# Optimization experiments

Measured on AMD Instinct MI355X. Metric: run time of the kernel, lower is better.

Reference implementation:

```python
import jax, jax.numpy as jnp
import numpy as np

ALPHA = 0.1          # loss decay rate along the hierarchy
H = 8                # hierarchy depth
NUM_CLASSES = 10000
NUM_NODES = 15000
BATCH = 1024


def setup_inputs() -> dict:
    key = jax.random.key(0)
    k1, k2, k3, k4 = jax.random.split(key, 4)
    logits = jax.random.normal(k1, (BATCH, NUM_CLASSES), dtype=jnp.float32)
    target_classes = jax.random.randint(k2, (BATCH,), 0, NUM_CLASSES)
    # L is an integer node/leaf matrix; values drawn in {1, 2} to avoid
    # division-by-zero in the module's num/den ratio (torch casts L to int).
    L = jax.random.randint(k3, (NUM_NODES, NUM_CLASSES), 1, 3)
    path_to_root = jax.random.randint(k4, (NUM_CLASSES, H), 0, NUM_NODES)
    return {"logits": logits, "target_classes": target_classes,
            "L": L, "path_to_root": path_to_root}


def reference(logits, target_classes, L, path_to_root):
    # Faithful to the torch forward, including the inner-loop index i
    # shadowing the batch index (logits rows 0..H-3 are used for every
    # sample). The unused log_softmax dead code is omitted.
    B = logits.shape[0]
    steps = H - 2
    paths = path_to_root[target_classes]                     # (B, H)
    lam = jnp.exp(-ALPHA * (H - jnp.arange(steps, dtype=logits.dtype) - 1.0))  # (steps,)
    Lf = L.astype(logits.dtype)
    # gather hierarchy rows for each sample/step: (B, steps, C)
    num = Lf[paths[:, :steps]] * logits[None, :steps, :]
    den = Lf[paths[:, 1:steps + 1]] * logits[None, :steps, :]
    terms = lam[None, :, None] * (num / den)                 # (B, steps, C)
    return -terms.sum(axis=(0, 1)) / B                       # (C,)
```

## Files before the change

kernel.cpp:

```cpp
#include <hip/hip_runtime.h>

#define ALPHA 0.1f
#define HDEPTH 8
#define STEPS 6
#define NCLASS 10000
#define NNODES 15000
#define BATCH 1024
#define NPAIRS (BATCH * STEPS)

#define PACK_STRIDE 320
#define NCOLS 313
#define NGROUPS 157
#define CHUNK 64
#define NCHUNKS (NPAIRS / CHUNK)

__global__ void build_pairs_kernel(const int* __restrict__ target,
                                   const int* __restrict__ path,
                                   int2* __restrict__ pairs,
                                   unsigned char* __restrict__ flags) {
    int p = blockIdx.x * blockDim.x + threadIdx.x;
    if (p >= NPAIRS) return;
    int s = p >> 10;
    int b = p & (BATCH - 1);
    int t = target[b];
    int n1 = path[t * HDEPTH + s];
    int n2 = path[t * HDEPTH + s + 1];
    pairs[p] = make_int2(n1, n2);
    flags[n1] = 1;
    flags[n2] = 1;
}

__global__ void __launch_bounds__(256)
pack_bits_kernel(const int* __restrict__ L,
                 const unsigned char* __restrict__ flags,
                 unsigned int* __restrict__ packed) {
    const int row = blockIdx.x;
    if (!flags[row]) return;
    const int wave = threadIdx.x >> 6;
    const int lane = threadIdx.x & 63;
    const int* Lrow = L + (size_t)row * NCLASS;
    unsigned long long* prow = (unsigned long long*)(packed + (size_t)row * PACK_STRIDE);
#pragma unroll 2
    for (int g = wave; g < NGROUPS; g += 4) {
        int c = g * 64 + lane;
        int v = (c < NCLASS) ? Lrow[c] : 1;
        unsigned long long m = __ballot(v == 2);
        if (lane == 0) prow[g] = m;
    }
}

__global__ void __launch_bounds__(320)
hce_bits_kernel(const unsigned int* __restrict__ packed,
                const int2* __restrict__ pairs,
                float* __restrict__ out) {
    __shared__ float part[320 * 33];
    const int col = threadIdx.x;
    const bool active = (col < NCOLS);
    const int p0 = blockIdx.x * CHUNK;
    const int s = p0 >> 10;
    const float w = expf(-ALPHA * (float)(HDEPTH - 1 - s));
    const float mult = -0.5f * w / (float)BATCH;

    unsigned int c2[32], cH[32];
#pragma unroll
    for (int k = 0; k < 32; ++k) { c2[k] = 0u; cH[k] = 0u; }

#pragma unroll 4
    for (int p = p0; p < p0 + CHUNK; ++p) {
        int2 pr = pairs[p];
        unsigned int wa = 0u, wb = 0u;
        if (active) {
            wa = packed[pr.x * PACK_STRIDE + col];
            wb = packed[pr.y * PACK_STRIDE + col];
        }
        unsigned int m2 = wa & ~wb;
        unsigned int mH = wb & ~wa;
#pragma unroll
        for (int k = 0; k < 32; ++k) {
            c2[k] += (m2 >> k) & 1u;
            cH[k] += (mH >> k) & 1u;
        }
    }

#pragma unroll
    for (int k = 0; k < 32; ++k) {
        int t = 2 * CHUNK + 2 * (int)c2[k] - (int)cH[k];
        part[col * 33 + k] = mult * (float)t;
    }
    __syncthreads();
    for (int c = col; c < NCLASS; c += 320) {
        atomicAdd(out + c, part[(c >> 5) * 33 + (c & 31)]);
    }
}

extern "C" void kernel_launch(void* const* d_in, const int* in_sizes, int n_in,
                              void* d_out, int out_size, void* d_ws, size_t ws_size,
                              hipStream_t stream) {
    const int* target = (const int*)d_in[1];
    const int* L      = (const int*)d_in[2];
    const int* path   = (const int*)d_in[3];
    float* out        = (float*)d_out;

    char* ws = (char*)d_ws;
    int2* pairs          = (int2*)ws;
    unsigned char* flags = (unsigned char*)(ws + 49152);
    unsigned int* packed = (unsigned int*)(ws + 65536);

    hipMemsetAsync(d_out, 0, NCLASS * sizeof(float), stream);
    hipMemsetAsync(flags, 0, NNODES, stream);

    build_pairs_kernel<<<(NPAIRS + 255) / 256, 256, 0, stream>>>(target, path, pairs, flags);
    pack_bits_kernel<<<NNODES, 256, 0, stream>>>(L, flags, packed);
    hce_bits_kernel<<<NCHUNKS, 320, 0, stream>>>(packed, pairs, out);
}
```

Before: 795.1 us.

## Use SWAR byte counters and two-stage partial reduction in bit-packed hierarchy loss

Packs L into bytes with vectorized int4 loads per thread instead of wave ballots. Replaces the 64 per-bit counters with 16 SWAR counters that hold four 8-bit lanes each, shrinks the pair chunk to 16 and tiles columns across a 2D grid. This cuts register pressure and raises block count. Per-chunk partials go to a workspace buffer and a separate reduce kernel sums them, replacing LDS staging and the heavy per-block atomics. The cost is extra global traffic for the partials and one more launch.

```diff
diff --git a/kernel.cpp b/kernel.cpp
--- a/kernel.cpp
+++ b/kernel.cpp
@@ -8,11 +8,18 @@
 #define BATCH 1024
 #define NPAIRS (BATCH * STEPS)
 
-#define PACK_STRIDE 320
+#define PACK_B 1280
+#define PACK_W 320
 #define NCOLS 313
-#define NGROUPS 157
-#define CHUNK 64
+
+#define CHUNK 16
 #define NCHUNKS (NPAIRS / CHUNK)
+#define PCLASS 10240
+#define COLTILE 128
+#define NTILES 3
+
+#define RSLICES 12
+#define RCHUNK (NCHUNKS / RSLICES)
 
 __global__ void build_pairs_kernel(const int* __restrict__ target,
                                    const int* __restrict__ path,
@@ -33,64 +40,99 @@
 __global__ void __launch_bounds__(256)
 pack_bits_kernel(const int* __restrict__ L,
                  const unsigned char* __restrict__ flags,
-                 unsigned int* __restrict__ packed) {
+                 unsigned char* __restrict__ packed) {
     const int row = blockIdx.x;
     if (!flags[row]) return;
-    const int wave = threadIdx.x >> 6;
-    const int lane = threadIdx.x & 63;
     const int* Lrow = L + (size_t)row * NCLASS;
-    unsigned long long* prow = (unsigned long long*)(packed + (size_t)row * PACK_STRIDE);
-#pragma unroll 2
-    for (int g = wave; g < NGROUPS; g += 4) {
-        int c = g * 64 + lane;
-        int v = (c < NCLASS) ? Lrow[c] : 1;
-        unsigned long long m = __ballot(v == 2);
-        if (lane == 0) prow[g] = m;
+    unsigned char* prow = packed + (size_t)row * PACK_B;
+#pragma unroll
+    for (int it = 0; it < 5; ++it) {
+        int jb = it * 256 + threadIdx.x;
+        unsigned int byte = 0u;
+        if (jb < 1250) {
+            const int4 a = *(const int4*)(Lrow + jb * 8);
+            const int4 b = *(const int4*)(Lrow + jb * 8 + 4);
+            byte  =  (unsigned)(a.x >> 1)
+                  | ((unsigned)(a.y >> 1) << 1)
+                  | ((unsigned)(a.z >> 1) << 2)
+                  | ((unsigned)(a.w >> 1) << 3)
+                  | ((unsigned)(b.x >> 1) << 4)
+                  | ((unsigned)(b.y >> 1) << 5)
+                  | ((unsigned)(b.z >> 1) << 6)
+                  | ((unsigned)(b.w >> 1) << 7);
+        }
+        prow[jb] = (unsigned char)byte;
     }
 }
 
-__global__ void __launch_bounds__(320)
+__global__ void __launch_bounds__(128)
 hce_bits_kernel(const unsigned int* __restrict__ packed,
                 const int2* __restrict__ pairs,
-                float* __restrict__ out) {
-    __shared__ float part[320 * 33];
-    const int col = threadIdx.x;
+                float* __restrict__ partial) {
+    const int chunk = blockIdx.x;
+    const int col = blockIdx.y * COLTILE + threadIdx.x;
     const bool active = (col < NCOLS);
-    const int p0 = blockIdx.x * CHUNK;
+    const int p0 = chunk * CHUNK;
     const int s = p0 >> 10;
-    const float w = expf(-ALPHA * (float)(HDEPTH - 1 - s));
+    const float w = __expf(-ALPHA * (float)(HDEPTH - 1 - s));
     const float mult = -0.5f * w / (float)BATCH;
 
-    unsigned int c2[32], cH[32];
+    unsigned int cp2[8], cpH[8];
 #pragma unroll
-    for (int k = 0; k < 32; ++k) { c2[k] = 0u; cH[k] = 0u; }
+    for (int k = 0; k < 8; ++k) { cp2[k] = 0u; cpH[k] = 0u; }
 
+    const int2* pp = pairs + p0;
 #pragma unroll 4
-    for (int p = p0; p < p0 + CHUNK; ++p) {
-        int2 pr = pairs[p];
+    for (int i = 0; i < CHUNK; ++i) {
+        int2 pr = pp[i];
         unsigned int wa = 0u, wb = 0u;
         if (active) {
-            wa = packed[pr.x * PACK_STRIDE + col];
-            wb = packed[pr.y * PACK_STRIDE + col];
+            wa = packed[(size_t)pr.x * PACK_W + col];
+            wb = packed[(size_t)pr.y * PACK_W + col];
         }
         unsigned int m2 = wa & ~wb;
         unsigned int mH = wb & ~wa;
 #pragma unroll
-        for (int k = 0; k < 32; ++k) {
-            c2[k] += (m2 >> k) & 1u;
-            cH[k] += (mH >> k) & 1u;
+        for (int k = 0; k < 8; ++k) {
+            cp2[k] += (m2 >> k) & 0x01010101u;
+            cpH[k] += (mH >> k) & 0x01010101u;
         }
     }
 
+    if (active) {
+        float v[32];
 #pragma unroll
-    for (int k = 0; k < 32; ++k) {
-        int t = 2 * CHUNK + 2 * (int)c2[k] - (int)cH[k];
-        part[col * 33 + k] = mult * (float)t;
+        for (int k = 0; k < 8; ++k) {
+#pragma unroll
+            for (int j = 0; j < 4; ++j) {
+                int c2 = (int)((cp2[k] >> (8 * j)) & 0xFFu);
+                int cH = (int)((cpH[k] >> (8 * j)) & 0xFFu);
+                v[k + 8 * j] = mult * (float)(2 * CHUNK + 2 * c2 - cH);
+            }
+        }
+        float4* dst = (float4*)(partial + (size_t)chunk * PCLASS + col * 32);
+#pragma unroll
+        for (int q = 0; q < 8; ++q)
+            dst[q] = make_float4(v[4*q], v[4*q+1], v[4*q+2], v[4*q+3]);
     }
-    __syncthreads();
-    for (int c = col; c < NCLASS; c += 320) {
-        atomicAdd(out + c, part[(c >> 5) * 33 + (c & 31)]);
+}
+
+__global__ void __launch_bounds__(256)
+reduce_kernel(const float4* __restrict__ partial, float* __restrict__ out) {
+    int c4 = blockIdx.x * 256 + threadIdx.x;
+    if (c4 >= NCLASS / 4) return;
+    int k0 = blockIdx.y * RCHUNK;
+    float4 s = make_float4(0.f, 0.f, 0.f, 0.f);
+#pragma unroll
+    for (int k = 0; k < RCHUNK; ++k) {
+        float4 v = partial[(size_t)(k0 + k) * (PCLASS / 4) + c4];
+        s.x += v.x; s.y += v.y; s.z += v.z; s.w += v.w;
     }
+    int c = c4 * 4;
+    atomicAdd(out + c + 0, s.x);
+    atomicAdd(out + c + 1, s.y);
+    atomicAdd(out + c + 2, s.z);
+    atomicAdd(out + c + 3, s.w);
 }
 
 extern "C" void kernel_launch(void* const* d_in, const int* in_sizes, int n_in,
@@ -102,14 +144,20 @@
     float* out        = (float*)d_out;
 
     char* ws = (char*)d_ws;
-    int2* pairs          = (int2*)ws;
-    unsigned char* flags = (unsigned char*)(ws + 49152);
-    unsigned int* packed = (unsigned int*)(ws + 65536);
+    int2* pairs           = (int2*)ws;
+    unsigned char* flags  = (unsigned char*)(ws + 49152);
+    unsigned char* packed = (unsigned char*)(ws + 65536);
+    float* partial        = (float*)(ws + 19267584);
 
     hipMemsetAsync(d_out, 0, NCLASS * sizeof(float), stream);
     hipMemsetAsync(flags, 0, NNODES, stream);
 
     build_pairs_kernel<<<(NPAIRS + 255) / 256, 256, 0, stream>>>(target, path, pairs, flags);
     pack_bits_kernel<<<NNODES, 256, 0, stream>>>(L, flags, packed);
-    hce_bits_kernel<<<NCHUNKS, 320, 0, stream>>>(packed, pairs, out);
+
+    dim3 gridC(NCHUNKS, NTILES);
+    hce_bits_kernel<<<gridC, COLTILE, 0, stream>>>((const unsigned int*)packed, pairs, partial);
+
+    dim3 gridR((NCLASS / 4 + 255) / 256, RSLICES);
+    reduce_kernel<<<gridR, 256, 0, stream>>>((const float4*)partial, out);
 }
```

Result: faster. 723.0 us (-9.1%).
